# Performance work log

Hardware: AMD Instinct MI355X
Metric: run time of the kernel (lower is better)

The kernel has to match this reference:

```python
import jax, jax.numpy as jnp
import numpy as np

N_NODES = 50000
N_EDGES = 800000
IN_DIM = 64
H_DIM = 64


def setup_inputs() -> dict:
    key = jax.random.key(0)
    ks = jax.random.split(key, 6)
    feat = jax.random.normal(ks[0], (N_NODES, IN_DIM), dtype=jnp.float32)
    W1 = jax.random.normal(ks[1], (IN_DIM, H_DIM), dtype=jnp.float32) * (1.0 / np.sqrt(IN_DIM))
    b1 = jnp.zeros((H_DIM,), dtype=jnp.float32)
    W2 = jax.random.normal(ks[2], (H_DIM, 1), dtype=jnp.float32) * (1.0 / np.sqrt(H_DIM))
    b2 = jnp.zeros((1,), dtype=jnp.float32)
    src = jax.random.randint(ks[3], (N_EDGES,), 0, N_NODES, dtype=jnp.int32)
    dst = jax.random.randint(ks[4], (N_EDGES,), 0, N_NODES, dtype=jnp.int32)
    return {"feat": feat, "W1": W1, "b1": b1, "W2": W2, "b2": b2, "src": src, "dst": dst}


def _norms(src, dst, n_nodes):
    # DGL GraphConv norm='both': symmetric D^{-1/2} A D^{-1/2}, degrees clamped to >=1
    ones = jnp.ones(src.shape[0], dtype=jnp.float32)
    out_deg = jax.ops.segment_sum(ones, src, num_segments=n_nodes)
    in_deg = jax.ops.segment_sum(ones, dst, num_segments=n_nodes)
    out_norm = jax.lax.rsqrt(jnp.clip(out_deg, 1.0))
    in_norm = jax.lax.rsqrt(jnp.clip(in_deg, 1.0))
    return out_norm, in_norm


def _graph_conv(feat, W, b, src, dst, out_norm, in_norm, act):
    h = feat * out_norm[:, None]          # scale source features by D_out^{-1/2}
    msg = h[src]                          # gather along edges [E, d]
    agg = jax.ops.segment_sum(msg, dst, num_segments=feat.shape[0])  # scatter-sum to dst
    agg = agg * in_norm[:, None]          # scale by D_in^{-1/2}
    return act(agg @ W + b)


def reference(feat, W1, b1, W2, b2, src, dst):
    out_norm, in_norm = _norms(src, dst, feat.shape[0])
    h = _graph_conv(feat, W1, b1, src, dst, out_norm, in_norm, jax.nn.relu)
    return _graph_conv(h, W2, b2, src, dst, out_norm, in_norm, jax.nn.sigmoid)
```

## Files before the change

kernel.cpp:

```cpp
#include <hip/hip_runtime.h>
#include <hip/hip_fp16.h>
#include <math.h>


#define BS 256
#define EPB 4096

__global__ void histA_featw1_kernel(const int* __restrict__ src, const int* __restrict__ dst,
                                    const float* __restrict__ feat, const float* __restrict__ W1,
                                    int* __restrict__ dstBinCount, int* __restrict__ srcBinCount,
                                    __half* __restrict__ featp,
                                    int E, int N, int NB, int T) {
    __shared__ float w[64 * 64];
    __shared__ int histD[256];
    __shared__ int histS[256];
    int tid = threadIdx.x;
    if ((int)blockIdx.x < T) {
        histD[tid] = 0; histS[tid] = 0;
        __syncthreads();
        int base = blockIdx.x * EPB;
        #pragma unroll
        for (int it = 0; it < EPB / BS; it++) {
            int e = base + it * BS + tid;
            if (e < E) {
                atomicAdd(&histD[dst[e] >> 8], 1);
                atomicAdd(&histS[src[e] >> 8], 1);
            }
        }
        __syncthreads();
        if (tid < NB) {
            if (histD[tid]) atomicAdd(&dstBinCount[tid], histD[tid]);
            if (histS[tid]) atomicAdd(&srcBinCount[tid], histS[tid]);
        }
    } else {
        for (int i = tid; i < 64 * 16; i += BS)
            ((float4*)w)[i] = ((const float4*)W1)[i];
        __syncthreads();
        int wave = tid >> 6, lane = tid & 63;
        int row = ((int)blockIdx.x - T) * 4 + wave;
        if (row >= N) return;
        const float4* fr = (const float4*)(feat + (size_t)row * 64);
        float acc = 0.0f;
        #pragma unroll
        for (int k4 = 0; k4 < 16; k4++) {
            float4 a = fr[k4];
            acc += a.x * w[(4 * k4 + 0) * 64 + lane];
            acc += a.y * w[(4 * k4 + 1) * 64 + lane];
            acc += a.z * w[(4 * k4 + 2) * 64 + lane];
            acc += a.w * w[(4 * k4 + 3) * 64 + lane];
        }
        featp[(size_t)row * 64 + lane] = __float2half(acc);
    }
}

__global__ void scan_bins_kernel(const int* __restrict__ dstBinCount, const int* __restrict__ srcBinCount,
                                 int* __restrict__ dstBinBase, int* __restrict__ srcBinBase,
                                 int* __restrict__ dstCursor, int* __restrict__ srcCursor, int NB) {
    __shared__ int s[256];
    int t = threadIdx.x;
    int v = (t < NB) ? dstBinCount[t] : 0;
    s[t] = v; __syncthreads();
    for (int off = 1; off < 256; off <<= 1) {
        int u = (t >= off) ? s[t - off] : 0; __syncthreads();
        s[t] += u; __syncthreads();
    }
    if (t < NB) {
        int ex = s[t] - v;
        dstBinBase[t] = ex; dstCursor[t] = ex;
        if (t == NB - 1) dstBinBase[NB] = s[t];
    }
    __syncthreads();
    v = (t < NB) ? srcBinCount[t] : 0;
    s[t] = v; __syncthreads();
    for (int off = 1; off < 256; off <<= 1) {
        int u = (t >= off) ? s[t - off] : 0; __syncthreads();
        s[t] += u; __syncthreads();
    }
    if (t < NB) {
        int ex = s[t] - v;
        srcBinBase[t] = ex; srcCursor[t] = ex;
        if (t == NB - 1) srcBinBase[NB] = s[t];
    }
}

__global__ void partition_kernel(const int* __restrict__ src, const int* __restrict__ dst,
                                 int* __restrict__ dstCursor, int* __restrict__ srcCursor,
                                 int* __restrict__ packed, int* __restrict__ srcPart,
                                 int E, int NB) {
    __shared__ int arr[256];
    int tid = threadIdx.x;
    int base = blockIdx.x * EPB;
    arr[tid] = 0; __syncthreads();
    #pragma unroll
    for (int it = 0; it < EPB / BS; it++) {
        int e = base + it * BS + tid;
        if (e < E) atomicAdd(&arr[dst[e] >> 8], 1);
    }
    __syncthreads();
    int h = arr[tid];
    int rb = (tid < NB && h) ? atomicAdd(&dstCursor[tid], h) : 0;
    __syncthreads();
    arr[tid] = rb;
    __syncthreads();
    #pragma unroll
    for (int it = 0; it < EPB / BS; it++) {
        int e = base + it * BS + tid;
        if (e < E) {
            int d = dst[e], s2 = src[e];
            int pos = atomicAdd(&arr[d >> 8], 1);
            packed[pos] = s2 | ((d & 255) << 17);
        }
    }
    __syncthreads();
    arr[tid] = 0; __syncthreads();
    #pragma unroll
    for (int it = 0; it < EPB / BS; it++) {
        int e = base + it * BS + tid;
        if (e < E) atomicAdd(&arr[src[e] >> 8], 1);
    }
    __syncthreads();
    h = arr[tid];
    rb = (tid < NB && h) ? atomicAdd(&srcCursor[tid], h) : 0;
    __syncthreads();
    arr[tid] = rb;
    __syncthreads();
    #pragma unroll
    for (int it = 0; it < EPB / BS; it++) {
        int e = base + it * BS + tid;
        if (e < E) {
            int s2 = src[e];
            int pos = atomicAdd(&arr[s2 >> 8], 1);
            srcPart[pos] = s2 & 255;
        }
    }
}

__global__ void finalize_kernel(const int* __restrict__ dstBinBase, const int* __restrict__ srcBinBase,
                                const int* __restrict__ packed, const int* __restrict__ srcPart,
                                int* __restrict__ csr_src, int* __restrict__ in_deg,
                                int* __restrict__ row_start, int* __restrict__ out_deg,
                                int N, int NB) {
    __shared__ int hist[256];
    __shared__ int sc[256];
    int tid = threadIdx.x;
    int b = blockIdx.x;
    if (b < NB) {
        int lo = dstBinBase[b], hi = dstBinBase[b + 1];
        hist[tid] = 0; __syncthreads();
        for (int i = lo + tid; i < hi; i += BS)
            atomicAdd(&hist[(packed[i] >> 17) & 255], 1);
        __syncthreads();
        int v = hist[tid];
        sc[tid] = v; __syncthreads();
        for (int off = 1; off < 256; off <<= 1) {
            int u = (tid >= off) ? sc[tid - off] : 0; __syncthreads();
            sc[tid] += u; __syncthreads();
        }
        int ex = sc[tid] - v;
        int n = b * 256 + tid;
        if (n < N) { in_deg[n] = v; row_start[n] = lo + ex; }
        sc[tid] = lo + ex;
        __syncthreads();
        for (int i = lo + tid; i < hi; i += BS) {
            int pv = packed[i];
            int pos = atomicAdd(&sc[(pv >> 17) & 255], 1);
            csr_src[pos] = pv & 0x1FFFF;
        }
    } else {
        int sb = b - NB;
        int lo = srcBinBase[sb], hi = srcBinBase[sb + 1];
        hist[tid] = 0; __syncthreads();
        for (int i = lo + tid; i < hi; i += BS)
            atomicAdd(&hist[srcPart[i]], 1);
        __syncthreads();
        int n = sb * 256 + tid;
        if (n < N) out_deg[n] = hist[tid];
    }
}

__global__ void csr_agg1_kernel(const int* __restrict__ row_start, const int* __restrict__ in_deg,
                                const int* __restrict__ csr_src, const int* __restrict__ out_deg,
                                const __half* __restrict__ featp,
                                const float* __restrict__ b1, const float* __restrict__ W2,
                                float* __restrict__ s_buf, int N) {
    int gid = blockIdx.x * blockDim.x + threadIdx.x;
    int n = gid >> 6;
    if (n >= N) return;
    int lane = threadIdx.x & 63;
    int g = lane >> 3;
    int l = lane & 7;
    int start = row_start[n];
    int deg = in_deg[n];
    float acc[8] = {0, 0, 0, 0, 0, 0, 0, 0};
    const uint4* fp4 = (const uint4*)featp;
    for (int j = 0; j < deg; j += 16) {
        int e0 = j + g;
        int e1 = j + 8 + g;
        bool p0 = e0 < deg;
        bool p1 = e1 < deg;
        int sn0 = p0 ? csr_src[start + e0] : 0;
        int sn1 = p1 ? csr_src[start + e1] : 0;
        uint4 q0 = {0, 0, 0, 0}, q1 = {0, 0, 0, 0};
        float on0 = 0.0f, on1 = 0.0f;
        if (p0) { q0 = fp4[(size_t)sn0 * 8 + l]; on0 = rsqrtf(fmaxf((float)out_deg[sn0], 1.0f)); }
        if (p1) { q1 = fp4[(size_t)sn1 * 8 + l]; on1 = rsqrtf(fmaxf((float)out_deg[sn1], 1.0f)); }
        const __half2* h0 = (const __half2*)&q0;
        const __half2* h1 = (const __half2*)&q1;
        #pragma unroll
        for (int c = 0; c < 4; c++) {
            float2 f0 = __half22float2(h0[c]);
            float2 f1 = __half22float2(h1[c]);
            acc[2 * c]     += on0 * f0.x + on1 * f1.x;
            acc[2 * c + 1] += on0 * f0.y + on1 * f1.y;
        }
    }
    #pragma unroll
    for (int off = 8; off < 64; off <<= 1) {
        #pragma unroll
        for (int c = 0; c < 8; c++)
            acc[c] += __shfl_xor(acc[c], off, 64);
    }
    float inn = rsqrtf(fmaxf((float)deg, 1.0f));
    float v = 0.0f;
    #pragma unroll
    for (int c = 0; c < 8; c++) {
        float h = fmaxf(inn * acc[c] + b1[l * 8 + c], 0.0f);
        v += h * W2[l * 8 + c];
    }
    #pragma unroll
    for (int off = 1; off < 8; off <<= 1)
        v += __shfl_xor(v, off, 64);
    if (lane == 0)
        s_buf[n] = rsqrtf(fmaxf((float)out_deg[n], 1.0f)) * v;
}

__global__ void csr_agg2_kernel(const int* __restrict__ row_start, const int* __restrict__ in_deg,
                                const int* __restrict__ csr_src,
                                const float* __restrict__ s_buf, const float* __restrict__ b2,
                                float* __restrict__ out, int N) {
    int gid = blockIdx.x * blockDim.x + threadIdx.x;
    int n = gid >> 4;
    if (n >= N) return;
    int sub = gid & 15;
    int start = row_start[n];
    int deg = in_deg[n];
    float a = 0.0f;
    for (int j = sub; j < deg; j += 32) {
        int j1 = j + 16;
        int i0 = csr_src[start + j];
        int i1 = (j1 < deg) ? csr_src[start + j1] : 0;
        float v0 = s_buf[i0];
        float v1 = (j1 < deg) ? s_buf[i1] : 0.0f;
        a += v0 + v1;
    }
    #pragma unroll
    for (int off = 1; off < 16; off <<= 1)
        a += __shfl_xor(a, off, 64);
    if (sub == 0) {
        float x = rsqrtf(fmaxf((float)deg, 1.0f)) * a + b2[0];
        out[n] = 1.0f / (1.0f + expf(-x));
    }
}

extern "C" void kernel_launch(void* const* d_in, const int* in_sizes, int n_in,
                              void* d_out, int out_size, void* d_ws, size_t ws_size,
                              hipStream_t stream) {
    const float* feat = (const float*)d_in[0];
    const float* W1   = (const float*)d_in[1];
    const float* b1   = (const float*)d_in[2];
    const float* W2   = (const float*)d_in[3];
    const float* b2   = (const float*)d_in[4];
    const int* src = (const int*)d_in[5];
    const int* dst = (const int*)d_in[6];
    float* out = (float*)d_out;

    const int N  = in_sizes[0] / 64;
    const int E  = in_sizes[5];
    const int NB = (N + 255) >> 8;
    const int T  = (E + EPB - 1) / EPB;

    int* wsi = (int*)d_ws;
    int* dstBinCount = wsi;
    int* srcBinCount = dstBinCount + NB;
    int* dstBinBase  = srcBinCount + NB;
    int* srcBinBase  = dstBinBase + NB + 1;
    int* dstCursor   = srcBinBase + NB + 1;
    int* srcCursor   = dstCursor + NB;
    int* in_deg      = srcCursor + NB;
    int* row_start   = in_deg + N;
    int* out_deg     = row_start + N;
    int* packed      = out_deg + N;
    int* srcPart     = packed + E;
    int* csr_src     = srcPart + E;
    size_t int_bytes = ((size_t)(6 * NB + 2) + 3 * (size_t)N + 3 * (size_t)E) * sizeof(int);
    size_t half_off  = (int_bytes + 15) & ~(size_t)15;
    __half* featp = (__half*)((char*)d_ws + half_off);
    float* s_buf  = (float*)((char*)d_ws + half_off + (size_t)64 * N * sizeof(__half));

    hipMemsetAsync(dstBinCount, 0, (size_t)2 * NB * sizeof(int), stream);

    histA_featw1_kernel<<<T + (N + 3) / 4, BS, 0, stream>>>(
        src, dst, feat, W1, dstBinCount, srcBinCount, featp, E, N, NB, T);
    scan_bins_kernel<<<1, 256, 0, stream>>>(
        dstBinCount, srcBinCount, dstBinBase, srcBinBase, dstCursor, srcCursor, NB);
    partition_kernel<<<T, BS, 0, stream>>>(
        src, dst, dstCursor, srcCursor, packed, srcPart, E, NB);
    finalize_kernel<<<2 * NB, BS, 0, stream>>>(
        dstBinBase, srcBinBase, packed, srcPart, csr_src, in_deg, row_start, out_deg, N, NB);
    csr_agg1_kernel<<<(int)(((size_t)N * 64 + BS - 1) / BS), BS, 0, stream>>>(
        row_start, in_deg, csr_src, out_deg, featp, b1, W2, s_buf, N);
    csr_agg2_kernel<<<(int)(((size_t)N * 16 + BS - 1) / BS), BS, 0, stream>>>(
        row_start, in_deg, csr_src, s_buf, b2, out, N);
}
```

Baseline: 185.6 us.

## Prescale projected features by out-norm and fuse partition histogram passes

The feature projection moves out of the histogram kernel into its own kernel that runs after the degrees are known. Each projected row is multiplied by its source rsqrt out-degree before being stored, so the aggregation loop no longer does a per-edge random out_deg gather and rsqrt. The partition kernel now reads src and dst once into registers and builds both bin histograms in a single pass, and srcPart is shrunk to bytes. In exchange the projection no longer overlaps with the histogram work, there is one extra launch, and register pressure in the partition kernel goes up.

```diff
diff --git a/kernel.cpp b/kernel.cpp
--- a/kernel.cpp
+++ b/kernel.cpp
@@ -6,50 +6,27 @@
 #define BS 256
 #define EPB 4096
 
-__global__ void histA_featw1_kernel(const int* __restrict__ src, const int* __restrict__ dst,
-                                    const float* __restrict__ feat, const float* __restrict__ W1,
-                                    int* __restrict__ dstBinCount, int* __restrict__ srcBinCount,
-                                    __half* __restrict__ featp,
-                                    int E, int N, int NB, int T) {
-    __shared__ float w[64 * 64];
+__global__ void hist_kernel(const int* __restrict__ src, const int* __restrict__ dst,
+                            int* __restrict__ dstBinCount, int* __restrict__ srcBinCount,
+                            int E, int NB) {
     __shared__ int histD[256];
     __shared__ int histS[256];
     int tid = threadIdx.x;
-    if ((int)blockIdx.x < T) {
-        histD[tid] = 0; histS[tid] = 0;
-        __syncthreads();
-        int base = blockIdx.x * EPB;
-        #pragma unroll
-        for (int it = 0; it < EPB / BS; it++) {
-            int e = base + it * BS + tid;
-            if (e < E) {
-                atomicAdd(&histD[dst[e] >> 8], 1);
-                atomicAdd(&histS[src[e] >> 8], 1);
-            }
-        }
-        __syncthreads();
-        if (tid < NB) {
-            if (histD[tid]) atomicAdd(&dstBinCount[tid], histD[tid]);
-            if (histS[tid]) atomicAdd(&srcBinCount[tid], histS[tid]);
-        }
-    } else {
-        for (int i = tid; i < 64 * 16; i += BS)
-            ((float4*)w)[i] = ((const float4*)W1)[i];
-        __syncthreads();
-        int wave = tid >> 6, lane = tid & 63;
-        int row = ((int)blockIdx.x - T) * 4 + wave;
-        if (row >= N) return;
-        const float4* fr = (const float4*)(feat + (size_t)row * 64);
-        float acc = 0.0f;
-        #pragma unroll
-        for (int k4 = 0; k4 < 16; k4++) {
-            float4 a = fr[k4];
-            acc += a.x * w[(4 * k4 + 0) * 64 + lane];
-            acc += a.y * w[(4 * k4 + 1) * 64 + lane];
-            acc += a.z * w[(4 * k4 + 2) * 64 + lane];
-            acc += a.w * w[(4 * k4 + 3) * 64 + lane];
-        }
-        featp[(size_t)row * 64 + lane] = __float2half(acc);
+    histD[tid] = 0; histS[tid] = 0;
+    __syncthreads();
+    int base = blockIdx.x * EPB;
+    #pragma unroll
+    for (int it = 0; it < EPB / BS; it++) {
+        int e = base + it * BS + tid;
+        if (e < E) {
+            atomicAdd(&histD[dst[e] >> 8], 1);
+            atomicAdd(&histS[src[e] >> 8], 1);
+        }
+    }
+    __syncthreads();
+    if (tid < NB) {
+        if (histD[tid]) atomicAdd(&dstBinCount[tid], histD[tid]);
+        if (histS[tid]) atomicAdd(&srcBinCount[tid], histS[tid]);
     }
 }
 
@@ -85,60 +62,47 @@
 
 __global__ void partition_kernel(const int* __restrict__ src, const int* __restrict__ dst,
                                  int* __restrict__ dstCursor, int* __restrict__ srcCursor,
-                                 int* __restrict__ packed, int* __restrict__ srcPart,
+                                 int* __restrict__ packed, unsigned char* __restrict__ srcPart,
                                  int E, int NB) {
-    __shared__ int arr[256];
+    __shared__ int curD[256];
+    __shared__ int curS[256];
     int tid = threadIdx.x;
     int base = blockIdx.x * EPB;
-    arr[tid] = 0; __syncthreads();
-    #pragma unroll
-    for (int it = 0; it < EPB / BS; it++) {
-        int e = base + it * BS + tid;
-        if (e < E) atomicAdd(&arr[dst[e] >> 8], 1);
-    }
-    __syncthreads();
-    int h = arr[tid];
-    int rb = (tid < NB && h) ? atomicAdd(&dstCursor[tid], h) : 0;
-    __syncthreads();
-    arr[tid] = rb;
+    int dv[EPB / BS], sv[EPB / BS];
+    curD[tid] = 0; curS[tid] = 0;
     __syncthreads();
     #pragma unroll
     for (int it = 0; it < EPB / BS; it++) {
         int e = base + it * BS + tid;
         if (e < E) {
-            int d = dst[e], s2 = src[e];
-            int pos = atomicAdd(&arr[d >> 8], 1);
+            dv[it] = dst[e]; sv[it] = src[e];
+            atomicAdd(&curD[dv[it] >> 8], 1);
+            atomicAdd(&curS[sv[it] >> 8], 1);
+        } else dv[it] = -1;
+    }
+    __syncthreads();
+    int hD = curD[tid], hS = curS[tid];
+    int rbD = (tid < NB && hD) ? atomicAdd(&dstCursor[tid], hD) : 0;
+    int rbS = (tid < NB && hS) ? atomicAdd(&srcCursor[tid], hS) : 0;
+    __syncthreads();
+    curD[tid] = rbD; curS[tid] = rbS;
+    __syncthreads();
+    #pragma unroll
+    for (int it = 0; it < EPB / BS; it++) {
+        if (dv[it] >= 0) {
+            int d = dv[it], s2 = sv[it];
+            int pos = atomicAdd(&curD[d >> 8], 1);
             packed[pos] = s2 | ((d & 255) << 17);
-        }
-    }
-    __syncthreads();
-    arr[tid] = 0; __syncthreads();
-    #pragma unroll
-    for (int it = 0; it < EPB / BS; it++) {
-        int e = base + it * BS + tid;
-        if (e < E) atomicAdd(&arr[src[e] >> 8], 1);
-    }
-    __syncthreads();
-    h = arr[tid];
-    rb = (tid < NB && h) ? atomicAdd(&srcCursor[tid], h) : 0;
-    __syncthreads();
-    arr[tid] = rb;
-    __syncthreads();
-    #pragma unroll
-    for (int it = 0; it < EPB / BS; it++) {
-        int e = base + it * BS + tid;
-        if (e < E) {
-            int s2 = src[e];
-            int pos = atomicAdd(&arr[s2 >> 8], 1);
-            srcPart[pos] = s2 & 255;
+            int pos2 = atomicAdd(&curS[s2 >> 8], 1);
+            srcPart[pos2] = (unsigned char)(s2 & 255);
         }
     }
 }
 
 __global__ void finalize_kernel(const int* __restrict__ dstBinBase, const int* __restrict__ srcBinBase,
-                                const int* __restrict__ packed, const int* __restrict__ srcPart,
+                                const int* __restrict__ packed, const unsigned char* __restrict__ srcPart,
                                 int* __restrict__ csr_src, int* __restrict__ in_deg,
-                                int* __restrict__ row_start, int* __restrict__ out_deg,
+                                int* __restrict__ row_start, float* __restrict__ out_norm,
                                 int N, int NB) {
     __shared__ int hist[256];
     __shared__ int sc[256];
@@ -174,14 +138,40 @@
             atomicAdd(&hist[srcPart[i]], 1);
         __syncthreads();
         int n = sb * 256 + tid;
-        if (n < N) out_deg[n] = hist[tid];
-    }
+        if (n < N) out_norm[n] = rsqrtf(fmaxf((float)hist[tid], 1.0f));
+    }
+}
+
+__global__ void featw1_kernel(const float* __restrict__ feat,
+                              const float* __restrict__ W1,
+                              const float* __restrict__ out_norm,
+                              __half* __restrict__ featp, int N) {
+    __shared__ float w[64 * 64];
+    int tid = threadIdx.x;
+    for (int i = tid; i < 64 * 16; i += BS)
+        ((float4*)w)[i] = ((const float4*)W1)[i];
+    __syncthreads();
+    int wave = tid >> 6, lane = tid & 63;
+    int row = blockIdx.x * 4 + wave;
+    if (row >= N) return;
+    const float4* fr = (const float4*)(feat + (size_t)row * 64);
+    float acc = 0.0f;
+    #pragma unroll
+    for (int k4 = 0; k4 < 16; k4++) {
+        float4 a = fr[k4];
+        acc += a.x * w[(4 * k4 + 0) * 64 + lane];
+        acc += a.y * w[(4 * k4 + 1) * 64 + lane];
+        acc += a.z * w[(4 * k4 + 2) * 64 + lane];
+        acc += a.w * w[(4 * k4 + 3) * 64 + lane];
+    }
+    featp[(size_t)row * 64 + lane] = __float2half(out_norm[row] * acc);
 }
 
 __global__ void csr_agg1_kernel(const int* __restrict__ row_start, const int* __restrict__ in_deg,
-                                const int* __restrict__ csr_src, const int* __restrict__ out_deg,
+                                const int* __restrict__ csr_src,
                                 const __half* __restrict__ featp,
                                 const float* __restrict__ b1, const float* __restrict__ W2,
+                                const float* __restrict__ out_norm,
                                 float* __restrict__ s_buf, int N) {
     int gid = blockIdx.x * blockDim.x + threadIdx.x;
     int n = gid >> 6;
@@ -201,17 +191,16 @@
         int sn0 = p0 ? csr_src[start + e0] : 0;
         int sn1 = p1 ? csr_src[start + e1] : 0;
         uint4 q0 = {0, 0, 0, 0}, q1 = {0, 0, 0, 0};
-        float on0 = 0.0f, on1 = 0.0f;
-        if (p0) { q0 = fp4[(size_t)sn0 * 8 + l]; on0 = rsqrtf(fmaxf((float)out_deg[sn0], 1.0f)); }
-        if (p1) { q1 = fp4[(size_t)sn1 * 8 + l]; on1 = rsqrtf(fmaxf((float)out_deg[sn1], 1.0f)); }
+        if (p0) q0 = fp4[(size_t)sn0 * 8 + l];
+        if (p1) q1 = fp4[(size_t)sn1 * 8 + l];
         const __half2* h0 = (const __half2*)&q0;
         const __half2* h1 = (const __half2*)&q1;
         #pragma unroll
         for (int c = 0; c < 4; c++) {
             float2 f0 = __half22float2(h0[c]);
             float2 f1 = __half22float2(h1[c]);
-            acc[2 * c]     += on0 * f0.x + on1 * f1.x;
-            acc[2 * c + 1] += on0 * f0.y + on1 * f1.y;
+            acc[2 * c]     += f0.x + f1.x;
+            acc[2 * c + 1] += f0.y + f1.y;
         }
     }
     #pragma unroll
@@ -231,7 +220,7 @@
     for (int off = 1; off < 8; off <<= 1)
         v += __shfl_xor(v, off, 64);
     if (lane == 0)
-        s_buf[n] = rsqrtf(fmaxf((float)out_deg[n], 1.0f)) * v;
+        s_buf[n] = out_norm[n] * v;
 }
 
 __global__ void csr_agg2_kernel(const int* __restrict__ row_start, const int* __restrict__ in_deg,
@@ -288,27 +277,27 @@
     int* srcCursor   = dstCursor + NB;
     int* in_deg      = srcCursor + NB;
     int* row_start   = in_deg + N;
-    int* out_deg     = row_start + N;
-    int* packed      = out_deg + N;
-    int* srcPart     = packed + E;
-    int* csr_src     = srcPart + E;
-    size_t int_bytes = ((size_t)(6 * NB + 2) + 3 * (size_t)N + 3 * (size_t)E) * sizeof(int);
-    size_t half_off  = (int_bytes + 15) & ~(size_t)15;
-    __half* featp = (__half*)((char*)d_ws + half_off);
-    float* s_buf  = (float*)((char*)d_ws + half_off + (size_t)64 * N * sizeof(__half));
+    int* packed      = row_start + N;
+    int* csr_src     = packed + E;
+    unsigned char* srcPart = (unsigned char*)(csr_src + E);
+    size_t off_b = ((size_t)(6 * NB + 2) + 2 * (size_t)N + 2 * (size_t)E) * sizeof(int) + (size_t)E;
+    off_b = (off_b + 15) & ~(size_t)15;
+    __half* featp   = (__half*)((char*)d_ws + off_b);
+    float*  out_norm = (float*)((char*)d_ws + off_b + (size_t)64 * N * sizeof(__half));
+    float*  s_buf    = out_norm + N;
 
     hipMemsetAsync(dstBinCount, 0, (size_t)2 * NB * sizeof(int), stream);
 
-    histA_featw1_kernel<<<T + (N + 3) / 4, BS, 0, stream>>>(
-        src, dst, feat, W1, dstBinCount, srcBinCount, featp, E, N, NB, T);
+    hist_kernel<<<T, BS, 0, stream>>>(src, dst, dstBinCount, srcBinCount, E, NB);
     scan_bins_kernel<<<1, 256, 0, stream>>>(
         dstBinCount, srcBinCount, dstBinBase, srcBinBase, dstCursor, srcCursor, NB);
     partition_kernel<<<T, BS, 0, stream>>>(
         src, dst, dstCursor, srcCursor, packed, srcPart, E, NB);
     finalize_kernel<<<2 * NB, BS, 0, stream>>>(
-        dstBinBase, srcBinBase, packed, srcPart, csr_src, in_deg, row_start, out_deg, N, NB);
+        dstBinBase, srcBinBase, packed, srcPart, csr_src, in_deg, row_start, out_norm, N, NB);
+    featw1_kernel<<<(N + 3) / 4, BS, 0, stream>>>(feat, W1, out_norm, featp, N);
     csr_agg1_kernel<<<(int)(((size_t)N * 64 + BS - 1) / BS), BS, 0, stream>>>(
-        row_start, in_deg, csr_src, out_deg, featp, b1, W2, s_buf, N);
+        row_start, in_deg, csr_src, featp, b1, W2, out_norm, s_buf, N);
     csr_agg2_kernel<<<(int)(((size_t)N * 16 + BS - 1) / BS), BS, 0, stream>>>(
         row_start, in_deg, csr_src, s_buf, b2, out, N);
 }
```

New measurement: 189.6 us. 2.2% more time.
